# Kernel tuning notes

Measured on AMD Instinct MI355X. Metric: run time of the kernel, lower is better.

Reference implementation:

```python
import jax, jax.numpy as jnp
import numpy as np
import math

DIM_EMB = 1024
DIM_QK = 1024
DIM_V = 1024
NORM_FACT = 1.0 / math.sqrt(DIM_EMB)

def setup_inputs() -> dict:
    key = jax.random.key(0)
    k0, k1, k2, k3 = jax.random.split(key, 4)
    x = jax.random.normal(k0, (4, 4096, DIM_EMB), dtype=jnp.float32)
    # nn.Linear weights are [out_features, in_features]; y = x @ W.T
    s = 1.0 / math.sqrt(DIM_EMB)
    Wq = jax.random.uniform(k1, (DIM_QK, DIM_EMB), jnp.float32, -s, s)
    Wk = jax.random.uniform(k2, (DIM_QK, DIM_EMB), jnp.float32, -s, s)
    Wv = jax.random.uniform(k3, (DIM_V, DIM_EMB), jnp.float32, -s, s)
    return {"x": x, "Wq": Wq, "Wk": Wk, "Wv": Wv}

def reference(x, Wq, Wk, Wv):
    # q,k,v: [b, n, d]
    q = jnp.einsum('bne,de->bnd', x, Wq)
    k = jnp.einsum('bne,de->bnd', x, Wk)
    v = jnp.einsum('bne,de->bnd', x, Wv)
    logits = jnp.einsum('bnd,bmd->bnm', q, k)  # [b, n, n]
    # Faithful to source: softmax over last dim FIRST, then scale by 1/sqrt(dim_embedding)
    score = jax.nn.softmax(logits, axis=-1) * NORM_FACT
    att = jnp.einsum('bnm,bmv->bnv', score, v)
    return att
```

## Files before the change

### kernel.cpp

```cpp
#include <hip/hip_runtime.h>
#include <hip/hip_bf16.h>

typedef _Float16 f16;
typedef _Float16 f16x4 __attribute__((ext_vector_type(4)));
typedef _Float16 f16x8 __attribute__((ext_vector_type(8)));
typedef float f32x4 __attribute__((ext_vector_type(4)));

__device__ __forceinline__ void gload16(const void* g, void* l) {
    __builtin_amdgcn_global_load_lds(
        (const __attribute__((address_space(1))) void*)g,
        (__attribute__((address_space(3))) void*)l, 16, 0, 0);
}

#define FENCE asm volatile("" ::: "memory")
#define BARRIER do { FENCE; __builtin_amdgcn_s_barrier(); FENCE; } while (0)

#define PHASE_MFMA(QI, QJ)                                                    \
    __builtin_amdgcn_s_setprio(1);                                            \
    _Pragma("unroll")                                                         \
    for (int ks = 0; ks < 2; ++ks)                                            \
      _Pragma("unroll")                                                       \
      for (int i = 0; i < 4; ++i)                                             \
        _Pragma("unroll")                                                     \
        for (int j = 0; j < 2; ++j)                                           \
          acc[(QI)*4 + i][(QJ)*2 + j] = __builtin_amdgcn_mfma_f32_16x16x32_f16( \
              a[i][ks], b[j][ks], acc[(QI)*4 + i][(QJ)*2 + j], 0, 0, 0);      \
    __builtin_amdgcn_s_setprio(0);

#define BT8_BODY(KBASE, NTILES)                                               \
    const int rr8 = lane >> 3;                                                \
    const int cs  = ((lane & 7) ^ rr8) << 3;                                  \
    const int ldsr = wid << 3;                                                \
    auto stageA = [&](int kt, int c, int h) {                                 \
        const size_t g0 = (size_t)(bm + (h << 7) + ldsr + rr8) * lda + (KBASE) + kt + cs; \
        gload16(A + g0,                      &sA[c][((h << 7) + ldsr) << 6]); \
        gload16(A + g0 + ((size_t)lda << 6), &sA[c][((h << 7) + 64 + ldsr) << 6]); \
    };                                                                        \
    auto stageB = [&](int kt, int c, int h) {                                 \
        const size_t g0 = (size_t)(bn + (h << 7) + ldsr + rr8) * ldb + (KBASE) + kt + cs; \
        gload16(B + g0,                      &sB[c][((h << 7) + ldsr) << 6]); \
        gload16(B + g0 + ((size_t)ldb << 6), &sB[c][((h << 7) + 64 + ldsr) << 6]); \
    };                                                                        \
    f32x4 acc[8][4] = {};                                                     \
    f16x8 a[4][2], b[2][2];                                                   \
    auto loadA = [&](int c, int qi) {                                         \
        _Pragma("unroll")                                                     \
        for (int i = 0; i < 4; ++i) {                                         \
            const int ra = wr * 128 + (qi * 4 + i) * 16 + (lane & 15);        \
            const int swz = (ra & 7) << 3;                                    \
            _Pragma("unroll")                                                 \
            for (int ks = 0; ks < 2; ++ks) {                                  \
                const int kk = ks * 32 + (lane >> 4) * 8;                     \
                a[i][ks] = *(const f16x8*)(&sA[c][(ra << 6) + (kk ^ swz)]);   \
            }                                                                 \
        }                                                                     \
    };                                                                        \
    auto loadB = [&](int c, int qj) {                                         \
        _Pragma("unroll")                                                     \
        for (int j = 0; j < 2; ++j) {                                         \
            const int rb = wc * 64 + (qj * 2 + j) * 16 + (lane & 15);         \
            const int swz = (rb & 7) << 3;                                    \
            _Pragma("unroll")                                                 \
            for (int ks = 0; ks < 2; ++ks) {                                  \
                const int kk = ks * 32 + (lane >> 4) * 8;                     \
                b[j][ks] = *(const f16x8*)(&sB[c][(rb << 6) + (kk ^ swz)]);   \
            }                                                                 \
        }                                                                     \
    };                                                                        \
    stageA(0, 0, 0); stageA(0, 0, 1); stageB(0, 0, 0); stageB(0, 0, 1);       \
    asm volatile("s_waitcnt vmcnt(0)" ::: "memory");                          \
    BARRIER;                                                                  \
    for (int g = 0; g < (NTILES); ++g) {                                      \
        const int c = g & 1, cn = c ^ 1;                                      \
        const int kn = (g + 1) << 6;                                          \
        const bool more = (g + 1) < (NTILES);                                 \
        loadA(c, 0); loadB(c, 0);                                             \
        if (more) { stageA(kn, cn, 0); stageA(kn, cn, 1); }                   \
        BARRIER; PHASE_MFMA(0, 0); BARRIER;                                   \
        loadB(c, 1);                                                          \
        if (more) { stageB(kn, cn, 0); stageB(kn, cn, 1); }                   \
        BARRIER; PHASE_MFMA(0, 1); BARRIER;                                   \
        loadA(c, 1); loadB(c, 0);                                             \
        BARRIER; PHASE_MFMA(1, 0); BARRIER;                                   \
        loadB(c, 1);                                                          \
        asm volatile("s_waitcnt vmcnt(0)" ::: "memory");                      \
        BARRIER; PHASE_MFMA(1, 1); BARRIER;                                   \
    }

template<bool F16OUT>
__global__ __launch_bounds__(512) void gemm_bt8(
    const f16* __restrict__ A, const f16* __restrict__ B, void* __restrict__ Cv,
    int K, int lda, int ldb, int ldc, float scale, int nbn)
{
    __shared__ f16 sA[2][256 * 64];
    __shared__ f16 sB[2][256 * 64];
    const int tid = threadIdx.x, lane = tid & 63, wid = tid >> 6;
    const int wr = wid >> 2, wc = wid & 3;
    const int cpx = gridDim.x >> 3;
    const int wg = (blockIdx.x & 7) * cpx + (blockIdx.x >> 3);
    const int bm = (wg / nbn) << 8, bn = (wg % nbn) << 8;

    BT8_BODY(0, K >> 6)

#pragma unroll
    for (int i = 0; i < 8; ++i)
#pragma unroll
        for (int j = 0; j < 4; ++j)
#pragma unroll
            for (int r = 0; r < 4; ++r) {
                const int row = bm + wr * 128 + i * 16 + ((lane >> 4) << 2) + r;
                const int col = bn + wc * 64 + j * 16 + (lane & 15);
                if constexpr (F16OUT)
                    ((f16*)Cv)[(size_t)row * ldc + col] = (f16)(acc[i][j][r] * scale);
                else
                    ((float*)Cv)[(size_t)row * ldc + col] = acc[i][j][r] * scale;
            }
}

__global__ __launch_bounds__(512) void gemm_pv8(
    const f16* __restrict__ A, const f16* __restrict__ B, float* __restrict__ Cout,
    f16* __restrict__ Pp, int lda, int ldb, float scale)
{
    __shared__ f16 sA[2][256 * 64];
    __shared__ f16 sB[2][256 * 64];
    const int tid = threadIdx.x, lane = tid & 63, wid = tid >> 6;
    const int wr = wid >> 2, wc = wid & 3;
    const int cpx = gridDim.x >> 3;
    const int wg = (blockIdx.x & 7) * cpx + (blockIdx.x >> 3);
    const int bm = (wg >> 2) << 8, bn = (wg & 3) << 8;
    const int z = blockIdx.y;
    const int kbase = z << 10;

    BT8_BODY(kbase, 16)

#pragma unroll
    for (int i = 0; i < 8; ++i)
#pragma unroll
        for (int j = 0; j < 4; ++j)
#pragma unroll
            for (int r = 0; r < 4; ++r) {
                const int row = bm + wr * 128 + i * 16 + ((lane >> 4) << 2) + r;
                const int col = bn + wc * 64 + j * 16 + (lane & 15);
                const float v = acc[i][j][r] * scale;
                if (z == 3) {
                    Cout[(size_t)row << 10 | col] = v;
                } else {
                    const size_t off = ((size_t)((z << 10) + (row >> 2)) << 13)
                                       + 4096 + ((row & 3) << 10) + col;
                    Pp[off] = (f16)v;
                }
            }
}

__global__ __launch_bounds__(256) void reduce_pv(
    float* __restrict__ Cout, const f16* __restrict__ Pp)
{
    const int i = blockIdx.x * 256 + threadIdx.x;
    const int r = i >> 7;
    const int c = (i & 127) << 3;
    const size_t base = ((size_t)(r >> 2) << 13) + 4096 + ((r & 3) << 10) + c;
    const f16x8 p0 = *(const f16x8*)(Pp + base);
    const f16x8 p1 = *(const f16x8*)(Pp + base + (1024LL << 13));
    const f16x8 p2 = *(const f16x8*)(Pp + base + (2048LL << 13));
    float* o = Cout + ((size_t)r << 10) + c;
    float4 o0 = *(float4*)o, o1 = *(float4*)(o + 4);
    o0.x += (float)p0[0] + (float)p1[0] + (float)p2[0];
    o0.y += (float)p0[1] + (float)p1[1] + (float)p2[1];
    o0.z += (float)p0[2] + (float)p1[2] + (float)p2[2];
    o0.w += (float)p0[3] + (float)p1[3] + (float)p2[3];
    o1.x += (float)p0[4] + (float)p1[4] + (float)p2[4];
    o1.y += (float)p0[5] + (float)p1[5] + (float)p2[5];
    o1.z += (float)p0[6] + (float)p1[6] + (float)p2[6];
    o1.w += (float)p0[7] + (float)p1[7] + (float)p2[7];
    *(float4*)o = o0;
    *(float4*)(o + 4) = o1;
}

template<bool F16IN, bool F16OUT, bool PIPE>
__global__ __launch_bounds__(256) void gemm_bt(
    const void* __restrict__ Av, const void* __restrict__ Bv, void* __restrict__ Cv,
    int K, int lda, int ldb, int ldc, float scale)
{
    constexpr int NB = PIPE ? 2 : 1;
    __shared__ f16 sA[NB][128 * 64];
    __shared__ f16 sB[NB][128 * 64];
    const int tid = threadIdx.x, lane = tid & 63, wid = tid >> 6;
    const int wr = wid >> 1, wc = wid & 1;
    const int bm = blockIdx.x * 128, bn = blockIdx.y * 128;

    f32x4 acc[4][4] = {};

    auto stage16 = [&](int kt, int bsel) {
        const f16* A = (const f16*)Av;
        const f16* B = (const f16*)Bv;
        const int rsub = lane >> 3;
        const int csw = ((lane & 7) ^ rsub) << 3;
#pragma unroll
        for (int i = 0; i < 4; ++i) {
            const int rb = (wid * 4 + i) * 8;
            gload16(A + (size_t)(bm + rb + rsub) * lda + kt + csw, &sA[bsel][rb * 64]);
            gload16(B + (size_t)(bn + rb + rsub) * ldb + kt + csw, &sB[bsel][rb * 64]);
        }
    };

    auto compute = [&](int bsel) {
#pragma unroll
        for (int ks = 0; ks < 2; ++ks) {
            const int kk = ks * 32 + (lane >> 4) * 8;
            f16x8 a[4], b[4];
#pragma unroll
            for (int i = 0; i < 4; ++i) {
                const int ra = wr * 64 + i * 16 + (lane & 15);
                a[i] = *(const f16x8*)(&sA[bsel][(ra << 6) + (kk ^ ((ra & 7) << 3))]);
                const int rb2 = wc * 64 + i * 16 + (lane & 15);
                b[i] = *(const f16x8*)(&sB[bsel][(rb2 << 6) + (kk ^ ((rb2 & 7) << 3))]);
            }
#pragma unroll
            for (int i = 0; i < 4; ++i)
#pragma unroll
                for (int j = 0; j < 4; ++j)
                    acc[i][j] = __builtin_amdgcn_mfma_f32_16x16x32_f16(a[i], b[j], acc[i][j], 0, 0, 0);
        }
    };

    if constexpr (PIPE) {
        stage16(0, 0);
        asm volatile("s_waitcnt vmcnt(0)" ::: "memory");
        __syncthreads();
        const int NT2 = K >> 6;
        for (int t = 0; t < NT2; ++t) {
            if (t + 1 < NT2) stage16((t + 1) << 6, (t + 1) & 1);
            compute(t & 1);
            asm volatile("s_waitcnt vmcnt(0)" ::: "memory");
            __builtin_amdgcn_s_barrier();
        }
    } else {
        for (int kt = 0; kt < K; kt += 64) {
            __syncthreads();
            stage16(kt, 0);
            __syncthreads();
            compute(0);
        }
    }
#pragma unroll
    for (int i = 0; i < 4; ++i)
#pragma unroll
        for (int j = 0; j < 4; ++j)
#pragma unroll
            for (int r = 0; r < 4; ++r) {
                const int row = bm + wr * 64 + i * 16 + (lane >> 4) * 4 + r;
                const int col = bn + wc * 64 + j * 16 + (lane & 15);
                if constexpr (F16OUT)
                    ((f16*)Cv)[(size_t)row * ldc + col] = (f16)acc[i][j][r];
                else
                    ((float*)Cv)[(size_t)row * ldc + col] = acc[i][j][r] * scale;
            }
}

__global__ __launch_bounds__(256) void cvt_f16(
    const float* __restrict__ s, f16* __restrict__ d, int n8)
{
    int i = blockIdx.x * 256 + threadIdx.x;
    const int stride = gridDim.x * 256;
    for (; i < n8; i += stride) {
        const float4 a = ((const float4*)s)[i * 2];
        const float4 b = ((const float4*)s)[i * 2 + 1];
        f16x8 o = { (f16)a.x, (f16)a.y, (f16)a.z, (f16)a.w,
                    (f16)b.x, (f16)b.y, (f16)b.z, (f16)b.w };
        ((f16x8*)d)[i] = o;
    }
}

__global__ __launch_bounds__(256) void softmax_inplace(float* S)
{
    const int lane = threadIdx.x & 63, wid = threadIdx.x >> 6;
    const int row = blockIdx.x * 4 + wid;
    float* src = S + (size_t)row * 4096;
    float4 v[16];
#pragma unroll
    for (int u = 0; u < 16; ++u)
        v[u] = ((const float4*)src)[u * 64 + lane];
    float m = -1e30f;
#pragma unroll
    for (int u = 0; u < 16; ++u)
        m = fmaxf(m, fmaxf(fmaxf(v[u].x, v[u].y), fmaxf(v[u].z, v[u].w)));
#pragma unroll
    for (int msk = 1; msk <= 32; msk <<= 1) m = fmaxf(m, __shfl_xor(m, msk));
    float s = 0.f;
#pragma unroll
    for (int u = 0; u < 16; ++u) {
        v[u].x = __expf(v[u].x - m); v[u].y = __expf(v[u].y - m);
        v[u].z = __expf(v[u].z - m); v[u].w = __expf(v[u].w - m);
        s += (v[u].x + v[u].y) + (v[u].z + v[u].w);
    }
#pragma unroll
    for (int msk = 1; msk <= 32; msk <<= 1) s += __shfl_xor(s, msk);
    const float inv = 1.0f / s;
    f16* dst = (f16*)S + (size_t)row * 8192;
#pragma unroll
    for (int u = 0; u < 16; ++u) {
        f16x4 p = { (f16)(v[u].x * inv), (f16)(v[u].y * inv),
                    (f16)(v[u].z * inv), (f16)(v[u].w * inv) };
        *(f16x4*)(dst + u * 256 + lane * 4) = p;
    }
}

extern "C" void kernel_launch(void* const* d_in, const int* in_sizes, int n_in,
                              void* d_out, int out_size, void* d_ws, size_t ws_size,
                              hipStream_t stream) {
    const float* x  = (const float*)d_in[0];
    const float* Wq = (const float*)d_in[1];
    const float* Wk = (const float*)d_in[2];
    const float* Wv = (const float*)d_in[3];
    float* out = (float*)d_out;

    f16*   qk  = (f16*)d_out;
    f16*   xh  = (f16*)d_ws;
    f16*   wqh = xh + 16384LL * 1024;
    f16*   wkh = wqh + 1024LL * 1024;
    float* Sf  = (float*)d_ws;
    f16*   Sh  = (f16*)d_ws;
    f16*   vTp = Sh + 3072LL * 8192 + 4096;

    cvt_f16<<<1024, 256, 0, stream>>>(x,  xh,  16384 * 1024 / 8);
    cvt_f16<<<512,  256, 0, stream>>>(Wq, wqh, 1024 * 1024 / 8);
    cvt_f16<<<512,  256, 0, stream>>>(Wk, wkh, 1024 * 1024 / 8);

    gemm_bt8<true><<<256, 512, 0, stream>>>(xh, wqh, qk,        1024, 1024, 1024, 2048, 1.f, 4);
    gemm_bt8<true><<<256, 512, 0, stream>>>(xh, wkh, qk + 1024, 1024, 1024, 1024, 2048, 1.f, 4);

    for (int b = 0; b < 4; ++b) {
        const size_t tb = (size_t)b * 4096;
        f16* xhb = (f16*)(out + tb * 1024);
        f16* wvh = xhb + 4096LL * 1024;
        gemm_bt8<false><<<256, 512, 0, stream>>>(
            qk + tb * 2048, qk + tb * 2048 + 1024, Sf,
            1024, 2048, 2048, 4096, 1.f, 16);
        softmax_inplace<<<1024, 256, 0, stream>>>(Sf);
        cvt_f16<<<1024, 256, 0, stream>>>(x + tb * 1024, xhb, 4096 * 1024 / 8);
        cvt_f16<<<512,  256, 0, stream>>>(Wv, wvh, 1024 * 1024 / 8);
        gemm_bt<true, true, true><<<dim3(8, 32), 256, 0, stream>>>(
            wvh, xhb, vTp, 1024, 1024, 1024, 8192, 1.f);
        gemm_pv8<<<dim3(64, 4), 512, 0, stream>>>(
            Sh, vTp, out + tb * 1024, Sh, 8192, 8192, 1.f / 32.f);
        reduce_pv<<<2048, 256, 0, stream>>>(out + tb * 1024, Sh);
    }
}
```

Before: 616.3 us.

## Fuse partial softmax into QK GEMM epilogue and rescale f16 probabilities afterward

The QK^T GEMM now computes per-tile row max and exp-sum in its epilogue and writes unnormalized f16 exponentials directly. A light rescale kernel combines the 16 tile statistics per row and applies the correction factor and the 1/32 scale in place. The old path wrote an fp32 score matrix and then ran a full softmax pass over it, so this removes that fp32 write and read. The cost is extra barriers and shuffles in the GEMM epilogue, plus f16 exponentials that may lose precision before rescaling. Workspace layouts for P, V^T and the split-K partials are repacked to match.

```diff
diff --git a/kernel.cpp b/kernel.cpp
--- a/kernel.cpp
+++ b/kernel.cpp
@@ -117,9 +117,109 @@
             }
 }
 
+__global__ __launch_bounds__(512) void gemm_qk(
+    const f16* __restrict__ A, const f16* __restrict__ B,
+    f16* __restrict__ P, float* __restrict__ mst, float* __restrict__ sst,
+    int lda, int ldb)
+{
+    __shared__ f16 sA[2][256 * 64];
+    __shared__ f16 sB[2][256 * 64];
+    const int tid = threadIdx.x, lane = tid & 63, wid = tid >> 6;
+    const int wr = wid >> 2, wc = wid & 3;
+    const int cpx = gridDim.x >> 3;
+    const int wg = (blockIdx.x & 7) * cpx + (blockIdx.x >> 3);
+    const int bm = (wg >> 4) << 8, bn = (wg & 15) << 8;
+
+    BT8_BODY(0, 16)
+
+    float* red = (float*)sA;
+    const int lg = lane >> 4;
+#pragma unroll
+    for (int i = 0; i < 8; ++i)
+#pragma unroll
+        for (int r = 0; r < 4; ++r) {
+            float v = fmaxf(fmaxf(acc[i][0][r], acc[i][1][r]),
+                            fmaxf(acc[i][2][r], acc[i][3][r]));
+#pragma unroll
+            for (int msk = 1; msk <= 8; msk <<= 1) v = fmaxf(v, __shfl_xor(v, msk));
+            if ((lane & 15) == 0) red[wr * 512 + (i * 16 + lg * 4 + r) * 4 + wc] = v;
+        }
+    BARRIER;
+    float mloc[8][4];
+#pragma unroll
+    for (int i = 0; i < 8; ++i)
+#pragma unroll
+        for (int r = 0; r < 4; ++r) {
+            const float4 q = *(const float4*)&red[wr * 512 + (i * 16 + lg * 4 + r) * 4];
+            mloc[i][r] = fmaxf(fmaxf(q.x, q.y), fmaxf(q.z, q.w));
+        }
+    BARRIER;
+#pragma unroll
+    for (int i = 0; i < 8; ++i)
+#pragma unroll
+        for (int r = 0; r < 4; ++r) {
+            float s = 0.f;
+#pragma unroll
+            for (int j = 0; j < 4; ++j) {
+                const float e = __expf(acc[i][j][r] - mloc[i][r]);
+                acc[i][j][r] = e; s += e;
+            }
+#pragma unroll
+            for (int msk = 1; msk <= 8; msk <<= 1) s += __shfl_xor(s, msk);
+            if ((lane & 15) == 0) red[wr * 512 + (i * 16 + lg * 4 + r) * 4 + wc] = s;
+        }
+    BARRIER;
+    const int t4 = bn >> 8;
+    if ((lane & 15) == 0) {
+#pragma unroll
+        for (int i = 0; i < 8; ++i)
+#pragma unroll
+            for (int r = 0; r < 4; ++r) {
+                const int row128 = i * 16 + lg * 4 + r;
+                const float4 q = *(const float4*)&red[wr * 512 + row128 * 4];
+                const int grow = bm + wr * 128 + row128;
+                mst[t4 * 4096 + grow] = mloc[i][r];
+                sst[t4 * 4096 + grow] = (q.x + q.y) + (q.z + q.w);
+            }
+    }
+#pragma unroll
+    for (int i = 0; i < 8; ++i)
+#pragma unroll
+        for (int j = 0; j < 4; ++j)
+#pragma unroll
+            for (int r = 0; r < 4; ++r) {
+                const int grow = bm + wr * 128 + i * 16 + lg * 4 + r;
+                const int gcol = bn + wc * 64 + j * 16 + (lane & 15);
+                P[(size_t)grow * 4096 + gcol] = (f16)acc[i][j][r];
+            }
+}
+
+__global__ __launch_bounds__(256) void scale_p(
+    f16* __restrict__ P, const float* __restrict__ mst, const float* __restrict__ sst)
+{
+    const int row = blockIdx.x;
+    float m = -1e30f;
+#pragma unroll
+    for (int t = 0; t < 16; ++t) m = fmaxf(m, mst[t * 4096 + row]);
+    float l = 0.f;
+#pragma unroll
+    for (int t = 0; t < 16; ++t) l += sst[t * 4096 + row] * __expf(mst[t * 4096 + row] - m);
+    const float inv = 1.0f / (32.0f * l);
+    const float f = __expf(mst[(threadIdx.x >> 4) * 4096 + row] - m) * inv;
+    f16* p = P + (size_t)row * 4096 + threadIdx.x * 16;
+    f16x8 va = *(f16x8*)p, vb = *(f16x8*)(p + 8);
+#pragma unroll
+    for (int u = 0; u < 8; ++u) {
+        va[u] = (f16)((float)va[u] * f);
+        vb[u] = (f16)((float)vb[u] * f);
+    }
+    *(f16x8*)p = va;
+    *(f16x8*)(p + 8) = vb;
+}
+
 __global__ __launch_bounds__(512) void gemm_pv8(
     const f16* __restrict__ A, const f16* __restrict__ B, float* __restrict__ Cout,
-    f16* __restrict__ Pp, int lda, int ldb, float scale)
+    f16* __restrict__ Pp, int lda, int ldb)
 {
     __shared__ f16 sA[2][256 * 64];
     __shared__ f16 sB[2][256 * 64];
@@ -141,14 +241,11 @@
             for (int r = 0; r < 4; ++r) {
                 const int row = bm + wr * 128 + i * 16 + ((lane >> 4) << 2) + r;
                 const int col = bn + wc * 64 + j * 16 + (lane & 15);
-                const float v = acc[i][j][r] * scale;
-                if (z == 3) {
-                    Cout[(size_t)row << 10 | col] = v;
-                } else {
-                    const size_t off = ((size_t)((z << 10) + (row >> 2)) << 13)
-                                       + 4096 + ((row & 3) << 10) + col;
-                    Pp[off] = (f16)v;
-                }
+                const float v = acc[i][j][r];
+                if (z == 3)
+                    Cout[((size_t)row << 10) + col] = v;
+                else
+                    Pp[(size_t)z * 4194304 + ((size_t)row << 10) + col] = (f16)v;
             }
 }
 
@@ -158,11 +255,11 @@
     const int i = blockIdx.x * 256 + threadIdx.x;
     const int r = i >> 7;
     const int c = (i & 127) << 3;
-    const size_t base = ((size_t)(r >> 2) << 13) + 4096 + ((r & 3) << 10) + c;
+    const size_t base = ((size_t)r << 10) + c;
     const f16x8 p0 = *(const f16x8*)(Pp + base);
-    const f16x8 p1 = *(const f16x8*)(Pp + base + (1024LL << 13));
-    const f16x8 p2 = *(const f16x8*)(Pp + base + (2048LL << 13));
-    float* o = Cout + ((size_t)r << 10) + c;
+    const f16x8 p1 = *(const f16x8*)(Pp + base + 4194304);
+    const f16x8 p2 = *(const f16x8*)(Pp + base + 8388608);
+    float* o = Cout + base;
     float4 o0 = *(float4*)o, o1 = *(float4*)(o + 4);
     o0.x += (float)p0[0] + (float)p1[0] + (float)p2[0];
     o0.y += (float)p0[1] + (float)p1[1] + (float)p2[1];
@@ -271,40 +368,6 @@
     }
 }
 
-__global__ __launch_bounds__(256) void softmax_inplace(float* S)
-{
-    const int lane = threadIdx.x & 63, wid = threadIdx.x >> 6;
-    const int row = blockIdx.x * 4 + wid;
-    float* src = S + (size_t)row * 4096;
-    float4 v[16];
-#pragma unroll
-    for (int u = 0; u < 16; ++u)
-        v[u] = ((const float4*)src)[u * 64 + lane];
-    float m = -1e30f;
-#pragma unroll
-    for (int u = 0; u < 16; ++u)
-        m = fmaxf(m, fmaxf(fmaxf(v[u].x, v[u].y), fmaxf(v[u].z, v[u].w)));
-#pragma unroll
-    for (int msk = 1; msk <= 32; msk <<= 1) m = fmaxf(m, __shfl_xor(m, msk));
-    float s = 0.f;
-#pragma unroll
-    for (int u = 0; u < 16; ++u) {
-        v[u].x = __expf(v[u].x - m); v[u].y = __expf(v[u].y - m);
-        v[u].z = __expf(v[u].z - m); v[u].w = __expf(v[u].w - m);
-        s += (v[u].x + v[u].y) + (v[u].z + v[u].w);
-    }
-#pragma unroll
-    for (int msk = 1; msk <= 32; msk <<= 1) s += __shfl_xor(s, msk);
-    const float inv = 1.0f / s;
-    f16* dst = (f16*)S + (size_t)row * 8192;
-#pragma unroll
-    for (int u = 0; u < 16; ++u) {
-        f16x4 p = { (f16)(v[u].x * inv), (f16)(v[u].y * inv),
-                    (f16)(v[u].z * inv), (f16)(v[u].w * inv) };
-        *(f16x4*)(dst + u * 256 + lane * 4) = p;
-    }
-}
-
 extern "C" void kernel_launch(void* const* d_in, const int* in_sizes, int n_in,
                               void* d_out, int out_size, void* d_ws, size_t ws_size,
                               hipStream_t stream) {
@@ -318,9 +381,12 @@
     f16*   xh  = (f16*)d_ws;
     f16*   wqh = xh + 16384LL * 1024;
     f16*   wkh = wqh + 1024LL * 1024;
-    float* Sf  = (float*)d_ws;
-    f16*   Sh  = (f16*)d_ws;
-    f16*   vTp = Sh + 3072LL * 8192 + 4096;
+
+    f16*   P   = (f16*)d_ws;
+    float* mst = (float*)((char*)d_ws + (32LL << 20));
+    float* sst = mst + 16 * 4096;
+    f16*   Pp  = (f16*)((char*)d_ws + (32LL << 20));
+    f16*   vTw = (f16*)((char*)d_ws + (56LL << 20));
 
     cvt_f16<<<1024, 256, 0, stream>>>(x,  xh,  16384 * 1024 / 8);
     cvt_f16<<<512,  256, 0, stream>>>(Wq, wqh, 1024 * 1024 / 8);
@@ -333,16 +399,15 @@
         const size_t tb = (size_t)b * 4096;
         f16* xhb = (f16*)(out + tb * 1024);
         f16* wvh = xhb + 4096LL * 1024;
-        gemm_bt8<false><<<256, 512, 0, stream>>>(
-            qk + tb * 2048, qk + tb * 2048 + 1024, Sf,
-            1024, 2048, 2048, 4096, 1.f, 16);
-        softmax_inplace<<<1024, 256, 0, stream>>>(Sf);
+        gemm_qk<<<256, 512, 0, stream>>>(
+            qk + tb * 2048, qk + tb * 2048 + 1024, P, mst, sst, 2048, 2048);
+        scale_p<<<4096, 256, 0, stream>>>(P, mst, sst);
         cvt_f16<<<1024, 256, 0, stream>>>(x + tb * 1024, xhb, 4096 * 1024 / 8);
         cvt_f16<<<512,  256, 0, stream>>>(Wv, wvh, 1024 * 1024 / 8);
         gemm_bt<true, true, true><<<dim3(8, 32), 256, 0, stream>>>(
-            wvh, xhb, vTp, 1024, 1024, 1024, 8192, 1.f);
+            wvh, xhb, vTw, 1024, 1024, 1024, 4096, 1.f);
         gemm_pv8<<<dim3(64, 4), 512, 0, stream>>>(
-            Sh, vTp, out + tb * 1024, Sh, 8192, 8192, 1.f / 32.f);
-        reduce_pv<<<2048, 256, 0, stream>>>(out + tb * 1024, Sh);
-    }
-}
+            P, vTw, out + tb * 1024, Pp, 4096, 4096);
+        reduce_pv<<<2048, 256, 0, stream>>>(out + tb * 1024, Pp);
+    }
+}
```

Measured after the change: 706.5 us. 14.6% more time.
